# Performance work log

Hardware: AMD Instinct MI355X
Metric: run time of the kernel (lower is better)

The kernel has to match this reference:

```python
import jax, jax.numpy as jnp
import numpy as np
from jax import lax

MU = 1.0  # Hopf bifurcation parameter (normal-form radial activation)

def hopf(s):
    # Hopf normal-form activation: f(s) = s * (mu - s^2)
    # (HopfBifur source not provided in repo snippet; this is the standard form.)
    return s * (MU - s * s)

def setup_inputs() -> dict:
    key = jax.random.key(0)
    k1, k2, k3 = jax.random.split(key, 3)
    B, T, D = 64, 1024, 512
    x = jax.random.normal(k1, (B, T, D), dtype=jnp.float32)
    # kernel / recurrent_kernel are real & imag parts of a unitary matrix in the
    # original init; random small weights suffice for a correctness baseline.
    scale = 1.0 / np.sqrt(D)
    kernel = jax.random.normal(k2, (D, D), dtype=jnp.float32) * scale
    recurrent_kernel = jax.random.normal(k3, (D, D), dtype=jnp.float32) * scale
    state0 = jnp.zeros((B, D), dtype=jnp.float32)
    return {"x": x, "kernel": kernel, "recurrent_kernel": recurrent_kernel, "state0": state0}

def reference(x, kernel, recurrent_kernel, state0):
    # x: [B, T, D]; recurrence: s_t = x_t @ K + s_{t-1} @ R; out_t = hopf(s_t)
    xs = jnp.swapaxes(x, 0, 1)  # [T, B, D]

    def step(s, xt):
        s_new = xt @ kernel + s @ recurrent_kernel  # [B, D]
        return s_new, hopf(s_new)

    _, outs = lax.scan(step, state0, xs)  # outs: [T, B, D]
    return jnp.swapaxes(outs, 0, 1)  # [B, T, D]
```

## Files before the change

### kernel.cpp

```cpp
#include <hip/hip_runtime.h>
#include <math.h>

#define NB      8
#define NBC     2
#define CHUNKS  64
#define LIM     0x1p100f
#define RESCALE_THRESH 0x1p44f
#define SCL_DN  0x1p-40f

#define BM 64
#define BN 64
#define BK 16

__global__ __launch_bounds__(256) void gemm_xk(const float* __restrict__ A,
                                               const float* __restrict__ B,
                                               float* __restrict__ C) {
    __shared__ float As[BK][BM + 4];
    __shared__ float Bs[BK][BN];

    const int tid  = threadIdx.x;
    const int col0 = blockIdx.x * BN;
    const int row0 = blockIdx.y * BM;

    const int tx = tid & 15;
    const int ty = tid >> 4;

    const int am = tid >> 2;
    const int ak = (tid & 3) << 2;
    const int bk  = tid >> 4;
    const int bn4 = (tid & 15) << 2;

    float acc[4][4] = {{0.f,0.f,0.f,0.f},{0.f,0.f,0.f,0.f},
                       {0.f,0.f,0.f,0.f},{0.f,0.f,0.f,0.f}};

    float4 av = *(const float4*)(A + (size_t)(row0 + am) * 512 + ak);
    float4 bv = *(const float4*)(B + (size_t)bk * 512 + (col0 + bn4));

    for (int k0 = 0; k0 < 512; k0 += BK) {
        __syncthreads();
        As[ak + 0][am] = av.x;
        As[ak + 1][am] = av.y;
        As[ak + 2][am] = av.z;
        As[ak + 3][am] = av.w;
        *(float4*)&Bs[bk][bn4] = bv;
        __syncthreads();
        if (k0 + BK < 512) {
            av = *(const float4*)(A + (size_t)(row0 + am) * 512 + (k0 + BK + ak));
            bv = *(const float4*)(B + (size_t)(k0 + BK + bk) * 512 + (col0 + bn4));
        }
#pragma unroll
        for (int k = 0; k < BK; ++k) {
            float4 a4 = *(const float4*)&As[k][ty << 2];
            float4 b4 = *(const float4*)&Bs[k][tx << 2];
            float ar[4] = {a4.x, a4.y, a4.z, a4.w};
            float br[4] = {b4.x, b4.y, b4.z, b4.w};
#pragma unroll
            for (int i = 0; i < 4; ++i)
#pragma unroll
                for (int j = 0; j < 4; ++j)
                    acc[i][j] = fmaf(ar[i], br[j], acc[i][j]);
        }
    }

#pragma unroll
    for (int i = 0; i < 4; ++i) {
        float4 v = make_float4(acc[i][0], acc[i][1], acc[i][2], acc[i][3]);
        *(float4*)(C + (size_t)(row0 + (ty << 2) + i) * 512 + col0 + (tx << 2)) = v;
    }
}

__global__ __launch_bounds__(256) void passA(const float* __restrict__ U,
                                             const float* __restrict__ R,
                                             float* __restrict__ y_end,
                                             int T, int B) {
    __shared__ float S[NB][512];
    const int g   = blockIdx.x;
    const int c   = blockIdx.y;
    const int tid = threadIdx.x;
    const int L   = T / CHUNKS;
    const int t0  = c * L;
    const int r0  = g * NB;
    const int j0  = tid;
    const int j1  = tid + 256;

#pragma unroll
    for (int r = 0; r < NB; ++r) { S[r][j0] = 0.f; S[r][j1] = 0.f; }
    __syncthreads();

    const float* __restrict__ R0 = R + j0;
    const float* __restrict__ R1 = R + j1;

    for (int t = t0; t < t0 + L; ++t) {
        float u0[NB], u1[NB];
#pragma unroll
        for (int r = 0; r < NB; ++r) {
            const float* Up = U + ((size_t)(r0 + r) * T + t) * 512;
            u0[r] = Up[j0];
            u1[r] = Up[j1];
        }
        float a0[NB] = {0.f,0.f,0.f,0.f,0.f,0.f,0.f,0.f};
        float a1[NB] = {0.f,0.f,0.f,0.f,0.f,0.f,0.f,0.f};
#pragma unroll 4
        for (int d = 0; d < 512; d += 4) {
            float p00 = R0[(size_t)(d + 0) * 512];
            float p01 = R0[(size_t)(d + 1) * 512];
            float p02 = R0[(size_t)(d + 2) * 512];
            float p03 = R0[(size_t)(d + 3) * 512];
            float p10 = R1[(size_t)(d + 0) * 512];
            float p11 = R1[(size_t)(d + 1) * 512];
            float p12 = R1[(size_t)(d + 2) * 512];
            float p13 = R1[(size_t)(d + 3) * 512];
#pragma unroll
            for (int r = 0; r < NB; ++r) {
                float4 s4 = *(const float4*)&S[r][d];
                a0[r] = fmaf(s4.x, p00, a0[r]);
                a0[r] = fmaf(s4.y, p01, a0[r]);
                a0[r] = fmaf(s4.z, p02, a0[r]);
                a0[r] = fmaf(s4.w, p03, a0[r]);
                a1[r] = fmaf(s4.x, p10, a1[r]);
                a1[r] = fmaf(s4.y, p11, a1[r]);
                a1[r] = fmaf(s4.z, p12, a1[r]);
                a1[r] = fmaf(s4.w, p13, a1[r]);
            }
        }
        __syncthreads();
#pragma unroll
        for (int r = 0; r < NB; ++r) {
            S[r][j0] = fminf(fmaxf(u0[r] + a0[r], -LIM), LIM);
            S[r][j1] = fminf(fmaxf(u1[r] + a1[r], -LIM), LIM);
        }
        __syncthreads();
    }

#pragma unroll
    for (int r = 0; r < NB; ++r) {
        y_end[((size_t)c * B + (r0 + r)) * 512 + j0] = S[r][j0];
        y_end[((size_t)c * B + (r0 + r)) * 512 + j1] = S[r][j1];
    }
}

__global__ __launch_bounds__(512) void combine(float* __restrict__ yeh,
                                               const float* __restrict__ s0,
                                               const float* __restrict__ RL,
                                               int* __restrict__ Eout,
                                               int B, int C) {
    __shared__ float S[NBC][512];
    __shared__ float red[8];
    const int g  = blockIdx.x;
    const int G  = gridDim.x;
    const int j  = threadIdx.x;
    const int r0 = g * NBC;

#pragma unroll
    for (int r = 0; r < NBC; ++r) {
        float v = s0[(size_t)(r0 + r) * 512 + j];
        S[r][j] = fminf(fmaxf(v, -LIM), LIM);
    }
    int E = 0;
    __syncthreads();

    const float* __restrict__ RLc = RL + j;

    for (int c = 1; c < C; ++c) {
        float acc[NBC] = {0.f, 0.f};
#pragma unroll 4
        for (int d = 0; d < 512; d += 4) {
            float rv0 = RLc[(size_t)(d + 0) * 512];
            float rv1 = RLc[(size_t)(d + 1) * 512];
            float rv2 = RLc[(size_t)(d + 2) * 512];
            float rv3 = RLc[(size_t)(d + 3) * 512];
#pragma unroll
            for (int r = 0; r < NBC; ++r) {
                float4 s4 = *(const float4*)&S[r][d];
                acc[r] = fmaf(s4.x, rv0, acc[r]);
                acc[r] = fmaf(s4.y, rv1, acc[r]);
                acc[r] = fmaf(s4.z, rv2, acc[r]);
                acc[r] = fmaf(s4.w, rv3, acc[r]);
            }
        }
        float us = ldexpf(1.f, -40 * E);
        float tmp[NBC];
        float mx = 0.f;
#pragma unroll
        for (int r = 0; r < NBC; ++r) {
            float ye = yeh[((size_t)(c - 1) * B + (r0 + r)) * 512 + j];
            float sn = fminf(fmaxf(fmaf(ye, us, acc[r]), -LIM), LIM);
            tmp[r] = sn;
            mx = fmaxf(mx, fabsf(sn));
        }
        float m = mx;
#pragma unroll
        for (int o = 32; o > 0; o >>= 1) m = fmaxf(m, __shfl_xor(m, o));
        if ((j & 63) == 0) red[j >> 6] = m;
        __syncthreads();
        m = fmaxf(fmaxf(fmaxf(red[0], red[1]), fmaxf(red[2], red[3])),
                  fmaxf(fmaxf(red[4], red[5]), fmaxf(red[6], red[7])));
        if (m > RESCALE_THRESH) {
#pragma unroll
            for (int r = 0; r < NBC; ++r) tmp[r] *= SCL_DN;
            E += 1;
        }
#pragma unroll
        for (int r = 0; r < NBC; ++r) {
            S[r][j] = tmp[r];
            yeh[((size_t)(c - 1) * B + (r0 + r)) * 512 + j] = tmp[r];
        }
        if (j == 0) Eout[c * G + g] = E;
        __syncthreads();
    }
}

__global__ __launch_bounds__(256) void passB(const float* __restrict__ R,
                                             const float* __restrict__ s0,
                                             const float* __restrict__ hbuf,
                                             const int* __restrict__ Ein,
                                             float* __restrict__ out,
                                             int T, int B, int Gc) {
    __shared__ float S[NB][512];
    __shared__ float red[4];
    const int g   = blockIdx.x;
    const int c   = blockIdx.y;
    const int tid = threadIdx.x;
    const int L   = T / CHUNKS;
    const int t0  = c * L;
    const int r0  = g * NB;
    const int j0  = tid;
    const int j1  = tid + 256;

    int E = 0;
    if (c == 0) {
#pragma unroll
        for (int r = 0; r < NB; ++r) {
            float v0 = s0[(size_t)(r0 + r) * 512 + j0];
            float v1 = s0[(size_t)(r0 + r) * 512 + j1];
            S[r][j0] = fminf(fmaxf(v0, -LIM), LIM);
            S[r][j1] = fminf(fmaxf(v1, -LIM), LIM);
        }
    } else {
        int Ep[NB / NBC];
        int Em = 0;
#pragma unroll
        for (int p = 0; p < NB / NBC; ++p) {
            Ep[p] = Ein[c * Gc + (r0 / NBC) + p];
            Em = (Ep[p] > Em) ? Ep[p] : Em;
        }
#pragma unroll
        for (int r = 0; r < NB; ++r) {
            int Er = Ep[r >> 1];
            float f = (Er == Em) ? 1.f : ldexpf(1.f, 40 * (Er - Em));
            float v0 = hbuf[((size_t)(c - 1) * B + (r0 + r)) * 512 + j0];
            float v1 = hbuf[((size_t)(c - 1) * B + (r0 + r)) * 512 + j1];
            S[r][j0] = v0 * f;
            S[r][j1] = v1 * f;
        }
        E = Em;
    }
    __syncthreads();

    double scaleE = ldexp(1.0, 40 * E);
    float  uscale = ldexpf(1.f, -40 * E);

    const float* __restrict__ R0 = R + j0;
    const float* __restrict__ R1 = R + j1;

    for (int t = t0; t < t0 + L; ++t) {
        float u0[NB], u1[NB];
        size_t oi0[NB];
#pragma unroll
        for (int r = 0; r < NB; ++r) {
            size_t base = ((size_t)(r0 + r) * T + t) * 512;
            oi0[r] = base;
            u0[r] = out[base + j0];
            u1[r] = out[base + j1];
        }
        float a0[NB] = {0.f,0.f,0.f,0.f,0.f,0.f,0.f,0.f};
        float a1[NB] = {0.f,0.f,0.f,0.f,0.f,0.f,0.f,0.f};
#pragma unroll 4
        for (int d = 0; d < 512; d += 4) {
            float p00 = R0[(size_t)(d + 0) * 512];
            float p01 = R0[(size_t)(d + 1) * 512];
            float p02 = R0[(size_t)(d + 2) * 512];
            float p03 = R0[(size_t)(d + 3) * 512];
            float p10 = R1[(size_t)(d + 0) * 512];
            float p11 = R1[(size_t)(d + 1) * 512];
            float p12 = R1[(size_t)(d + 2) * 512];
            float p13 = R1[(size_t)(d + 3) * 512];
#pragma unroll
            for (int r = 0; r < NB; ++r) {
                float4 s4 = *(const float4*)&S[r][d];
                a0[r] = fmaf(s4.x, p00, a0[r]);
                a0[r] = fmaf(s4.y, p01, a0[r]);
                a0[r] = fmaf(s4.z, p02, a0[r]);
                a0[r] = fmaf(s4.w, p03, a0[r]);
                a1[r] = fmaf(s4.x, p10, a1[r]);
                a1[r] = fmaf(s4.y, p11, a1[r]);
                a1[r] = fmaf(s4.z, p12, a1[r]);
                a1[r] = fmaf(s4.w, p13, a1[r]);
            }
        }
        float s0n[NB], s1n[NB];
        float mx = 0.f;
#pragma unroll
        for (int r = 0; r < NB; ++r) {
            float v0 = fminf(fmaxf(fmaf(u0[r], uscale, a0[r]), -LIM), LIM);
            float v1 = fminf(fmaxf(fmaf(u1[r], uscale, a1[r]), -LIM), LIM);
            s0n[r] = v0; s1n[r] = v1;
            mx = fmaxf(mx, fmaxf(fabsf(v0), fabsf(v1)));
            double sd0 = (double)v0 * scaleE;
            double ov0 = sd0 * (1.0 - sd0 * sd0);
            double oc0 = fmin(fmax(ov0, -3.0e38), 3.0e38);
            oc0 = (oc0 == oc0) ? oc0 : 0.0;
            out[oi0[r] + j0] = (float)oc0;
            double sd1 = (double)v1 * scaleE;
            double ov1 = sd1 * (1.0 - sd1 * sd1);
            double oc1 = fmin(fmax(ov1, -3.0e38), 3.0e38);
            oc1 = (oc1 == oc1) ? oc1 : 0.0;
            out[oi0[r] + j1] = (float)oc1;
        }
        if ((t & 7) == 7) {
            float m = mx;
#pragma unroll
            for (int o = 32; o > 0; o >>= 1) m = fmaxf(m, __shfl_xor(m, o));
            if ((tid & 63) == 0) red[tid >> 6] = m;
            __syncthreads();
            m = fmaxf(fmaxf(red[0], red[1]), fmaxf(red[2], red[3]));
            if (m > RESCALE_THRESH) {
#pragma unroll
                for (int r = 0; r < NB; ++r) { s0n[r] *= SCL_DN; s1n[r] *= SCL_DN; }
                E += 1;
                scaleE *= 0x1p40;
                uscale *= SCL_DN;
            }
        } else {
            __syncthreads();
        }
#pragma unroll
        for (int r = 0; r < NB; ++r) {
            S[r][j0] = s0n[r];
            S[r][j1] = s1n[r];
        }
        __syncthreads();
    }
}

__global__ __launch_bounds__(512) void recur(const float* __restrict__ R,
                                             const float* __restrict__ s0,
                                             float* __restrict__ out,
                                             int T) {
    __shared__ float sbuf[2][512];
    __shared__ float red[512];

    const int b = blockIdx.x;
    const int j = threadIdx.x;

    float sini = s0[(size_t)b * 512 + j];
    sbuf[0][j] = fminf(fmaxf(sini, -LIM), LIM);
    __syncthreads();

    const float* __restrict__ Rc = R + j;
    float* __restrict__ ob = out + (size_t)b * T * 512;

    int cur = 0;
    double scaleE = 1.0;
    float  uscale = 1.0f;

    for (int t = 0; t < T; ++t) {
        const float* s = sbuf[cur];
        float d0 = 0.f, d1 = 0.f, d2 = 0.f, d3 = 0.f;
#pragma unroll 8
        for (int d = 0; d < 512; d += 4) {
            d0 = fmaf(s[d + 0], Rc[(size_t)(d + 0) * 512], d0);
            d1 = fmaf(s[d + 1], Rc[(size_t)(d + 1) * 512], d1);
            d2 = fmaf(s[d + 2], Rc[(size_t)(d + 2) * 512], d2);
            d3 = fmaf(s[d + 3], Rc[(size_t)(d + 3) * 512], d3);
        }
        float u = ob[(size_t)t * 512 + j];
        float snew = fmaf(u, uscale, (d0 + d1) + (d2 + d3));
        snew = fminf(fmaxf(snew, -LIM), LIM);

        double sd = (double)snew * scaleE;
        double ov = sd * (1.0 - sd * sd);
        double oc = fmin(fmax(ov, -3.0e38), 3.0e38);
        oc = (oc == oc) ? oc : 0.0;
        ob[(size_t)t * 512 + j] = (float)oc;

        if ((t & 31) == 31) {
            red[j] = fabsf(snew);
            __syncthreads();
#pragma unroll
            for (int w = 256; w > 0; w >>= 1) {
                if (j < w) red[j] = fmaxf(red[j], red[j + w]);
                __syncthreads();
            }
            float m = red[0];
            __syncthreads();
            if (m > RESCALE_THRESH) {
                snew   *= SCL_DN;
                scaleE *= 0x1p40;
                uscale *= SCL_DN;
            }
        }

        sbuf[cur ^ 1][j] = snew;
        __syncthreads();
        cur ^= 1;
    }
}

extern "C" void kernel_launch(void* const* d_in, const int* in_sizes, int n_in,
                              void* d_out, int out_size, void* d_ws, size_t ws_size,
                              hipStream_t stream) {
    const float* x  = (const float*)d_in[0];
    const float* K  = (const float*)d_in[1];
    const float* R  = (const float*)d_in[2];
    const float* s0 = (const float*)d_in[3];
    float* out = (float*)d_out;

    const int D = 512;
    const int M = in_sizes[0] / D;
    const int B = in_sizes[3] / D;
    const int T = M / B;
    const int G  = B / NB;
    const int Gc = B / NBC;

    gemm_xk<<<dim3(D / BN, M / BM), 256, 0, stream>>>(x, K, out);

    const size_t MB = 1u << 20;
    const size_t slot = (size_t)B * D * sizeof(float);
    const size_t off_RLa = 0;
    const size_t off_RLb = 1 * MB;
    const size_t off_yeh = 2 * MB;
    const size_t off_E   = off_yeh + (size_t)(CHUNKS - 1) * slot;
    const size_t need    = off_yeh + (size_t)CHUNKS * slot;

    if (ws_size < need || (T % CHUNKS) != 0 || (B % NB) != 0 || (B % NBC) != 0 ||
        D != 512 || (size_t)CHUNKS * Gc * sizeof(int) > slot) {
        recur<<<B, D, 0, stream>>>(R, s0, out, T);
        return;
    }

    char* ws = (char*)d_ws;
    float* RLa  = (float*)(ws + off_RLa);
    float* RLb  = (float*)(ws + off_RLb);
    float* yeh  = (float*)(ws + off_yeh);
    int*   Ebuf = (int*)(ws + off_E);

    dim3 sq(D / BN, D / BM);
    gemm_xk<<<sq, 256, 0, stream>>>(R,   R,   RLa);
    gemm_xk<<<sq, 256, 0, stream>>>(RLa, RLa, RLb);
    gemm_xk<<<sq, 256, 0, stream>>>(RLb, RLb, RLa);
    gemm_xk<<<sq, 256, 0, stream>>>(RLa, RLa, RLb);

    passA<<<dim3(G, CHUNKS - 1), 256, 0, stream>>>(out, R, yeh, T, B);

    combine<<<Gc, 512, 0, stream>>>(yeh, s0, RLb, Ebuf, B, CHUNKS);

    passB<<<dim3(G, CHUNKS), 256, 0, stream>>>(R, s0, yeh, Ebuf, out, T, B, Gc);
}
```

Before: 3.001 ms.

## Split recurrent matvec K dimension across thread pairs with shuffle reduction

In passA and passB, each thread pair now splits the 512-long reduction dimension in half, and each thread computes 4 output columns instead of 2, combining partial sums with a lane-xor shuffle. The intent is to raise register reuse of each R element and each shared-memory S read per FMA, so the per-step matvec spends less time on loads. It adds shuffle and select overhead and more accumulator registers, which could lower occupancy. Each R load is also strided by 128 columns, which may hurt coalescing.

```diff
diff --git a/kernel.cpp b/kernel.cpp
--- a/kernel.cpp
+++ b/kernel.cpp
@@ -74,68 +74,79 @@
                                              float* __restrict__ y_end,
                                              int T, int B) {
     __shared__ float S[NB][512];
-    const int g   = blockIdx.x;
-    const int c   = blockIdx.y;
-    const int tid = threadIdx.x;
-    const int L   = T / CHUNKS;
-    const int t0  = c * L;
-    const int r0  = g * NB;
-    const int j0  = tid;
-    const int j1  = tid + 256;
-
-#pragma unroll
-    for (int r = 0; r < NB; ++r) { S[r][j0] = 0.f; S[r][j1] = 0.f; }
+    const int g    = blockIdx.x;
+    const int c    = blockIdx.y;
+    const int tid  = threadIdx.x;
+    const int half = tid & 1;
+    const int cq   = tid >> 1;
+    const int d0   = half << 8;
+    const int jw0  = cq + (half << 8);
+    const int jw1  = jw0 + 128;
+    const int L    = T / CHUNKS;
+    const int t0   = c * L;
+    const int r0   = g * NB;
+
+#pragma unroll
+    for (int r = 0; r < NB; ++r) { S[r][jw0] = 0.f; S[r][jw1] = 0.f; }
     __syncthreads();
-
-    const float* __restrict__ R0 = R + j0;
-    const float* __restrict__ R1 = R + j1;
 
     for (int t = t0; t < t0 + L; ++t) {
         float u0[NB], u1[NB];
 #pragma unroll
         for (int r = 0; r < NB; ++r) {
             const float* Up = U + ((size_t)(r0 + r) * T + t) * 512;
-            u0[r] = Up[j0];
-            u1[r] = Up[j1];
-        }
-        float a0[NB] = {0.f,0.f,0.f,0.f,0.f,0.f,0.f,0.f};
-        float a1[NB] = {0.f,0.f,0.f,0.f,0.f,0.f,0.f,0.f};
-#pragma unroll 4
-        for (int d = 0; d < 512; d += 4) {
-            float p00 = R0[(size_t)(d + 0) * 512];
-            float p01 = R0[(size_t)(d + 1) * 512];
-            float p02 = R0[(size_t)(d + 2) * 512];
-            float p03 = R0[(size_t)(d + 3) * 512];
-            float p10 = R1[(size_t)(d + 0) * 512];
-            float p11 = R1[(size_t)(d + 1) * 512];
-            float p12 = R1[(size_t)(d + 2) * 512];
-            float p13 = R1[(size_t)(d + 3) * 512];
+            u0[r] = Up[jw0];
+            u1[r] = Up[jw1];
+        }
+        float acc[NB][4];
+#pragma unroll
+        for (int r = 0; r < NB; ++r)
+#pragma unroll
+            for (int cc = 0; cc < 4; ++cc) acc[r][cc] = 0.f;
+
+        for (int dd = 0; dd < 256; dd += 4) {
+            const int d = d0 + dd;
+            const float* __restrict__ Rd = R + (size_t)d * 512 + cq;
+            float rv[4][4];
+#pragma unroll
+            for (int kk = 0; kk < 4; ++kk)
+#pragma unroll
+                for (int cc = 0; cc < 4; ++cc)
+                    rv[kk][cc] = Rd[(size_t)kk * 512 + cc * 128];
 #pragma unroll
             for (int r = 0; r < NB; ++r) {
                 float4 s4 = *(const float4*)&S[r][d];
-                a0[r] = fmaf(s4.x, p00, a0[r]);
-                a0[r] = fmaf(s4.y, p01, a0[r]);
-                a0[r] = fmaf(s4.z, p02, a0[r]);
-                a0[r] = fmaf(s4.w, p03, a0[r]);
-                a1[r] = fmaf(s4.x, p10, a1[r]);
-                a1[r] = fmaf(s4.y, p11, a1[r]);
-                a1[r] = fmaf(s4.z, p12, a1[r]);
-                a1[r] = fmaf(s4.w, p13, a1[r]);
-            }
-        }
-        __syncthreads();
-#pragma unroll
-        for (int r = 0; r < NB; ++r) {
-            S[r][j0] = fminf(fmaxf(u0[r] + a0[r], -LIM), LIM);
-            S[r][j1] = fminf(fmaxf(u1[r] + a1[r], -LIM), LIM);
-        }
+#pragma unroll
+                for (int cc = 0; cc < 4; ++cc) {
+                    acc[r][cc] = fmaf(s4.x, rv[0][cc], acc[r][cc]);
+                    acc[r][cc] = fmaf(s4.y, rv[1][cc], acc[r][cc]);
+                    acc[r][cc] = fmaf(s4.z, rv[2][cc], acc[r][cc]);
+                    acc[r][cc] = fmaf(s4.w, rv[3][cc], acc[r][cc]);
+                }
+            }
+        }
+        float sn0[NB], sn1[NB];
+#pragma unroll
+        for (int r = 0; r < NB; ++r) {
+            float gv0 = half ? acc[r][0] : acc[r][2];
+            float gv1 = half ? acc[r][1] : acc[r][3];
+            float rc0 = __shfl_xor(gv0, 1);
+            float rc1 = __shfl_xor(gv1, 1);
+            float a0 = (half ? acc[r][2] : acc[r][0]) + rc0;
+            float a1 = (half ? acc[r][3] : acc[r][1]) + rc1;
+            sn0[r] = fminf(fmaxf(u0[r] + a0, -LIM), LIM);
+            sn1[r] = fminf(fmaxf(u1[r] + a1, -LIM), LIM);
+        }
+        __syncthreads();
+#pragma unroll
+        for (int r = 0; r < NB; ++r) { S[r][jw0] = sn0[r]; S[r][jw1] = sn1[r]; }
         __syncthreads();
     }
 
 #pragma unroll
     for (int r = 0; r < NB; ++r) {
-        y_end[((size_t)c * B + (r0 + r)) * 512 + j0] = S[r][j0];
-        y_end[((size_t)c * B + (r0 + r)) * 512 + j1] = S[r][j1];
+        y_end[((size_t)c * B + (r0 + r)) * 512 + jw0] = S[r][jw0];
+        y_end[((size_t)c * B + (r0 + r)) * 512 + jw1] = S[r][jw1];
     }
 }
 
@@ -218,23 +229,26 @@
                                              int T, int B, int Gc) {
     __shared__ float S[NB][512];
     __shared__ float red[4];
-    const int g   = blockIdx.x;
-    const int c   = blockIdx.y;
-    const int tid = threadIdx.x;
-    const int L   = T / CHUNKS;
-    const int t0  = c * L;
-    const int r0  = g * NB;
-    const int j0  = tid;
-    const int j1  = tid + 256;
+    const int g    = blockIdx.x;
+    const int c    = blockIdx.y;
+    const int tid  = threadIdx.x;
+    const int half = tid & 1;
+    const int cq   = tid >> 1;
+    const int d0   = half << 8;
+    const int jw0  = cq + (half << 8);
+    const int jw1  = jw0 + 128;
+    const int L    = T / CHUNKS;
+    const int t0   = c * L;
+    const int r0   = g * NB;
 
     int E = 0;
     if (c == 0) {
 #pragma unroll
         for (int r = 0; r < NB; ++r) {
-            float v0 = s0[(size_t)(r0 + r) * 512 + j0];
-            float v1 = s0[(size_t)(r0 + r) * 512 + j1];
-            S[r][j0] = fminf(fmaxf(v0, -LIM), LIM);
-            S[r][j1] = fminf(fmaxf(v1, -LIM), LIM);
+            float v0 = s0[(size_t)(r0 + r) * 512 + jw0];
+            float v1 = s0[(size_t)(r0 + r) * 512 + jw1];
+            S[r][jw0] = fminf(fmaxf(v0, -LIM), LIM);
+            S[r][jw1] = fminf(fmaxf(v1, -LIM), LIM);
         }
     } else {
         int Ep[NB / NBC];
@@ -248,10 +262,10 @@
         for (int r = 0; r < NB; ++r) {
             int Er = Ep[r >> 1];
             float f = (Er == Em) ? 1.f : ldexpf(1.f, 40 * (Er - Em));
-            float v0 = hbuf[((size_t)(c - 1) * B + (r0 + r)) * 512 + j0];
-            float v1 = hbuf[((size_t)(c - 1) * B + (r0 + r)) * 512 + j1];
-            S[r][j0] = v0 * f;
-            S[r][j1] = v1 * f;
+            float v0 = hbuf[((size_t)(c - 1) * B + (r0 + r)) * 512 + jw0];
+            float v1 = hbuf[((size_t)(c - 1) * B + (r0 + r)) * 512 + jw1];
+            S[r][jw0] = v0 * f;
+            S[r][jw1] = v1 * f;
         }
         E = Em;
     }
@@ -260,62 +274,67 @@
     double scaleE = ldexp(1.0, 40 * E);
     float  uscale = ldexpf(1.f, -40 * E);
 
-    const float* __restrict__ R0 = R + j0;
-    const float* __restrict__ R1 = R + j1;
-
     for (int t = t0; t < t0 + L; ++t) {
         float u0[NB], u1[NB];
-        size_t oi0[NB];
+        size_t ob[NB];
 #pragma unroll
         for (int r = 0; r < NB; ++r) {
             size_t base = ((size_t)(r0 + r) * T + t) * 512;
-            oi0[r] = base;
-            u0[r] = out[base + j0];
-            u1[r] = out[base + j1];
-        }
-        float a0[NB] = {0.f,0.f,0.f,0.f,0.f,0.f,0.f,0.f};
-        float a1[NB] = {0.f,0.f,0.f,0.f,0.f,0.f,0.f,0.f};
-#pragma unroll 4
-        for (int d = 0; d < 512; d += 4) {
-            float p00 = R0[(size_t)(d + 0) * 512];
-            float p01 = R0[(size_t)(d + 1) * 512];
-            float p02 = R0[(size_t)(d + 2) * 512];
-            float p03 = R0[(size_t)(d + 3) * 512];
-            float p10 = R1[(size_t)(d + 0) * 512];
-            float p11 = R1[(size_t)(d + 1) * 512];
-            float p12 = R1[(size_t)(d + 2) * 512];
-            float p13 = R1[(size_t)(d + 3) * 512];
+            ob[r] = base;
+            u0[r] = out[base + jw0];
+            u1[r] = out[base + jw1];
+        }
+        float acc[NB][4];
+#pragma unroll
+        for (int r = 0; r < NB; ++r)
+#pragma unroll
+            for (int cc = 0; cc < 4; ++cc) acc[r][cc] = 0.f;
+
+        for (int dd = 0; dd < 256; dd += 4) {
+            const int d = d0 + dd;
+            const float* __restrict__ Rd = R + (size_t)d * 512 + cq;
+            float rv[4][4];
+#pragma unroll
+            for (int kk = 0; kk < 4; ++kk)
+#pragma unroll
+                for (int cc = 0; cc < 4; ++cc)
+                    rv[kk][cc] = Rd[(size_t)kk * 512 + cc * 128];
 #pragma unroll
             for (int r = 0; r < NB; ++r) {
                 float4 s4 = *(const float4*)&S[r][d];
-                a0[r] = fmaf(s4.x, p00, a0[r]);
-                a0[r] = fmaf(s4.y, p01, a0[r]);
-                a0[r] = fmaf(s4.z, p02, a0[r]);
-                a0[r] = fmaf(s4.w, p03, a0[r]);
-                a1[r] = fmaf(s4.x, p10, a1[r]);
-                a1[r] = fmaf(s4.y, p11, a1[r]);
-                a1[r] = fmaf(s4.z, p12, a1[r]);
-                a1[r] = fmaf(s4.w, p13, a1[r]);
-            }
-        }
-        float s0n[NB], s1n[NB];
+#pragma unroll
+                for (int cc = 0; cc < 4; ++cc) {
+                    acc[r][cc] = fmaf(s4.x, rv[0][cc], acc[r][cc]);
+                    acc[r][cc] = fmaf(s4.y, rv[1][cc], acc[r][cc]);
+                    acc[r][cc] = fmaf(s4.z, rv[2][cc], acc[r][cc]);
+                    acc[r][cc] = fmaf(s4.w, rv[3][cc], acc[r][cc]);
+                }
+            }
+        }
+        float sn0[NB], sn1[NB];
         float mx = 0.f;
 #pragma unroll
         for (int r = 0; r < NB; ++r) {
-            float v0 = fminf(fmaxf(fmaf(u0[r], uscale, a0[r]), -LIM), LIM);
-            float v1 = fminf(fmaxf(fmaf(u1[r], uscale, a1[r]), -LIM), LIM);
-            s0n[r] = v0; s1n[r] = v1;
+            float gv0 = half ? acc[r][0] : acc[r][2];
+            float gv1 = half ? acc[r][1] : acc[r][3];
+            float rc0 = __shfl_xor(gv0, 1);
+            float rc1 = __shfl_xor(gv1, 1);
+            float a0 = (half ? acc[r][2] : acc[r][0]) + rc0;
+            float a1 = (half ? acc[r][3] : acc[r][1]) + rc1;
+            float v0 = fminf(fmaxf(fmaf(u0[r], uscale, a0), -LIM), LIM);
+            float v1 = fminf(fmaxf(fmaf(u1[r], uscale, a1), -LIM), LIM);
+            sn0[r] = v0; sn1[r] = v1;
             mx = fmaxf(mx, fmaxf(fabsf(v0), fabsf(v1)));
             double sd0 = (double)v0 * scaleE;
             double ov0 = sd0 * (1.0 - sd0 * sd0);
             double oc0 = fmin(fmax(ov0, -3.0e38), 3.0e38);
             oc0 = (oc0 == oc0) ? oc0 : 0.0;
-            out[oi0[r] + j0] = (float)oc0;
+            out[ob[r] + jw0] = (float)oc0;
             double sd1 = (double)v1 * scaleE;
             double ov1 = sd1 * (1.0 - sd1 * sd1);
             double oc1 = fmin(fmax(ov1, -3.0e38), 3.0e38);
             oc1 = (oc1 == oc1) ? oc1 : 0.0;
-            out[oi0[r] + j1] = (float)oc1;
+            out[ob[r] + jw1] = (float)oc1;
         }
         if ((t & 7) == 7) {
             float m = mx;
@@ -326,7 +345,7 @@
             m = fmaxf(fmaxf(red[0], red[1]), fmaxf(red[2], red[3]));
             if (m > RESCALE_THRESH) {
 #pragma unroll
-                for (int r = 0; r < NB; ++r) { s0n[r] *= SCL_DN; s1n[r] *= SCL_DN; }
+                for (int r = 0; r < NB; ++r) { sn0[r] *= SCL_DN; sn1[r] *= SCL_DN; }
                 E += 1;
                 scaleE *= 0x1p40;
                 uscale *= SCL_DN;
@@ -336,8 +355,8 @@
         }
 #pragma unroll
         for (int r = 0; r < NB; ++r) {
-            S[r][j0] = s0n[r];
-            S[r][j1] = s1n[r];
+            S[r][jw0] = sn0[r];
+            S[r][jw1] = sn1[r];
         }
         __syncthreads();
     }
```

New measurement: 3.357 ms. 11.9% more time.
